# Kernel optimization log

Hardware: AMD Instinct MI355X
Metric: run time of the kernel (lower is better)

Reference implementation:

```python
import jax, jax.numpy as jnp
import numpy as np

K = 3  # kernel_dim
PAD = 1


def setup_inputs() -> dict:
    key = jax.random.key(0)
    ks = jax.random.split(key, 7)
    B, C_in, C_out, R = 2, 32, 64, 64
    H = W = D = 64
    return {
        "x": jax.random.normal(ks[0], (B, C_in, H, W, D), dtype=jnp.float32),
        "U_k_h": jax.random.normal(ks[1], (K, R), dtype=jnp.float32),
        "U_k_w": jax.random.normal(ks[2], (K, R), dtype=jnp.float32),
        "U_k_d": jax.random.normal(ks[3], (K, R), dtype=jnp.float32),
        "U_c_in": jax.random.normal(ks[4], (C_in, R), dtype=jnp.float32),
        "U_c_out": jax.random.normal(ks[5], (R, C_out), dtype=jnp.float32),
        "bias": jax.random.normal(ks[6], (C_out,), dtype=jnp.float32),
    }


def _cpd_conv3d(x, U_k_h, U_k_w, U_k_d, U_c_in, U_c_out, bias):
    # Equivalent to: patches[b,c,h,w,d,kh,kw,kd] contracted with
    # U_c_in[c,r] U_k_h[kh,r] U_k_w[kw,r] U_k_d[kd,r] U_c_out[r,co]
    # -> out[b,co,h,w,d].  We exploit the CP (rank-separable) structure
    # instead of materializing the unfolded patch tensor.
    xp = jnp.pad(x, ((0, 0), (0, 0), (PAD, PAD), (PAD, PAD), (PAD, PAD)))
    # channel contraction: [B, R, H+2, W+2, D+2]
    t = jnp.einsum('bchwd,cr->brhwd', xp, U_c_in)
    B, R, Hp, Wp, Dp = t.shape
    H, W, D = Hp - 2 * PAD, Wp - 2 * PAD, Dp - 2 * PAD
    # separable kernel contractions (fixed K=3 unrolled loops)
    t = sum(t[:, :, k:k + H, :, :] * U_k_h[k][None, :, None, None, None] for k in range(K))
    t = sum(t[:, :, :, k:k + W, :] * U_k_w[k][None, :, None, None, None] for k in range(K))
    t = sum(t[:, :, :, :, k:k + D] * U_k_d[k][None, :, None, None, None] for k in range(K))
    out = jnp.einsum('brhwd,rc->bchwd', t, U_c_out)
    return out + bias[None, :, None, None, None]


def reference(x, U_k_h, U_k_w, U_k_d, U_c_in, U_c_out, bias):
    return _cpd_conv3d(x, U_k_h, U_k_w, U_k_d, U_c_in, U_c_out, bias)
```

## Files before the change

kernel.cpp:

```cpp
#include <hip/hip_runtime.h>
#include <hip/hip_bf16.h>

typedef __attribute__((ext_vector_type(8))) short short8;
typedef __attribute__((ext_vector_type(4))) float f32x4;

__device__ __forceinline__ float b2f(short s) {
    return __uint_as_float(((unsigned int)(unsigned short)s) << 16);
}
__device__ __forceinline__ float b2f_lo(unsigned u) {
    return __uint_as_float(u << 16);
}
__device__ __forceinline__ float b2f_hi(unsigned u) {
    return __uint_as_float(u & 0xffff0000u);
}
__device__ __forceinline__ short f2b(float f) {
    union { __hip_bfloat16 h; short s; } cv;
    cv.h = __float2bfloat16(f);
    return cv.s;
}
__device__ __forceinline__ unsigned pack2(float a, float b) {
    union { __hip_bfloat162 h; unsigned u; } cv;
    cv.h = __float22bfloat162_rn(make_float2(a, b));
    return cv.u;
}

__global__ __launch_bounds__(64)
void k0_prep(const float* __restrict__ Uco, const float* __restrict__ Ucin,
             short* __restrict__ ucotT, short* __restrict__ ucinT)
{
    const int i = blockIdx.x * 64 + threadIdx.x;
    if (i < 4096) {
        int co = i >> 6, r = i & 63;
        ucotT[co * 64 + r] = f2b(Uco[r * 64 + co]);
    } else {
        int j = i - 4096;
        int r = j >> 5, c = j & 31;
        ucinT[r * 32 + c] = f2b(Ucin[c * 64 + r]);
    }
}

__global__ __launch_bounds__(256)
void k1_channel(const float* __restrict__ x,
                const float* __restrict__ Ucin,
                const short* __restrict__ ucinT_g,
                short* __restrict__ t)
{
    __shared__ short xs[256 * 32];
    __shared__ short uci[64 * 32];

    const int tid = threadIdx.x;
    const int gp0 = blockIdx.x * 256;
    const int b   = gp0 >> 18;
    const int sp  = (gp0 & 262143) + tid;
    const float* xp = x + ((long)b << 23) + sp;

    if (ucinT_g) {
        ((short8*)uci)[tid] = ((const short8*)ucinT_g)[tid];
    } else {
        for (int i = tid; i < 2048; i += 256) {
            int r = i >> 5, c = i & 31;
            uci[i] = f2b(Ucin[c * 64 + r]);
        }
    }

    {
        float v[32];
#pragma unroll
        for (int c = 0; c < 32; ++c) v[c] = xp[(long)c << 18];
        const int swz = (tid >> 1) & 3;
#pragma unroll
        for (int oct = 0; oct < 4; ++oct) {
            uint4 o;
            o.x = pack2(v[oct * 8 + 0], v[oct * 8 + 1]);
            o.y = pack2(v[oct * 8 + 2], v[oct * 8 + 3]);
            o.z = pack2(v[oct * 8 + 4], v[oct * 8 + 5]);
            o.w = pack2(v[oct * 8 + 6], v[oct * 8 + 7]);
            *(uint4*)&xs[tid * 32 + ((oct ^ swz) << 3)] = o;
        }
    }
    __syncthreads();

    const int lane = tid & 63, wv = tid >> 6;
    const int l15 = lane & 15, quad = lane >> 4;

    short8 afr[4];
#pragma unroll
    for (int mt = 0; mt < 4; ++mt)
        afr[mt] = *(const short8*)&uci[(mt * 16 + l15) * 32 + quad * 8];

    f32x4 acc[4][4] = {};
#pragma unroll
    for (int nt = 0; nt < 4; ++nt) {
        const int srow = wv * 64 + nt * 16 + l15;
        const int slot = quad ^ ((srow >> 1) & 3);
        short8 bfr = *(const short8*)&xs[srow * 32 + (slot << 3)];
#pragma unroll
        for (int mt = 0; mt < 4; ++mt)
            acc[mt][nt] = __builtin_amdgcn_mfma_f32_16x16x32_bf16(
                afr[mt], bfr, acc[mt][nt], 0, 0, 0);
    }

#pragma unroll
    for (int nt = 0; nt < 4; ++nt) {
        const int srow = wv * 64 + nt * 16 + l15;
        short* tb = t + ((size_t)(gp0 + srow) << 6);
#pragma unroll
        for (int mt = 0; mt < 4; ++mt) {
            uint2 o;
            o.x = pack2(acc[mt][nt][0], acc[mt][nt][1]);
            o.y = pack2(acc[mt][nt][2], acc[mt][nt][3]);
            *(uint2*)&tb[mt * 16 + quad * 4] = o;
        }
    }
}

__global__ __launch_bounds__(256)
void k2_conv_gemm(const short* __restrict__ t,
                  const float* __restrict__ Ukh,
                  const float* __restrict__ Ukw,
                  const float* __restrict__ Ukd,
                  const float* __restrict__ Uco,
                  const float* __restrict__ bias,
                  const short* __restrict__ ucotT,
                  float* __restrict__ out)
{
    __shared__ short s[66 * 64];
    __shared__ short p[64 * 72];
    __shared__ short ucot[64 * 72];

    const int tid = threadIdx.x;

    const int bid  = blockIdx.x;
    const int slot = bid & 7;
    const int idx  = bid >> 3;
    const int b    = idx >> 9;
    const int rem  = idx & 511;
    const int h    = slot * 8 + (rem >> 6);
    const int w    = rem & 63;

    const short* colp[9];
    bool valid[9];
#pragma unroll
    for (int kh = 0; kh < 3; ++kh) {
#pragma unroll
        for (int kw = 0; kw < 3; ++kw) {
            int hh = h + kh - 1, ww = w + kw - 1;
            bool v = ((unsigned)hh < 64u) && ((unsigned)ww < 64u);
            valid[kh * 3 + kw] = v;
            long base = v ? ((long)(b * 262144 + hh * 4096 + ww * 64) << 6) : 0;
            colp[kh * 3 + kw] = t + base;
        }
    }

    if (ucotT) {
        for (int i = tid; i < 512; i += 256) {
            int co = i >> 3, rb = i & 7;
            short8 v = *(const short8*)&ucotT[co * 64 + rb * 8];
            *(short8*)&ucot[co * 72 + rb * 8] = v;
        }
    } else {
        for (int i = tid; i < 4096; i += 256) {
            int r = i >> 6, co = i & 63;
            ucot[co * 72 + r] = f2b(Uco[i]);
        }
    }

    const int rq = tid & 15;
    float4 W[9];
    {
        float4 a[3], c[3];
#pragma unroll
        for (int k = 0; k < 3; ++k) {
            a[k] = *(const float4*)&Ukh[k * 64 + 4 * rq];
            c[k] = *(const float4*)&Ukw[k * 64 + 4 * rq];
        }
#pragma unroll
        for (int kh = 0; kh < 3; ++kh)
#pragma unroll
            for (int kw = 0; kw < 3; ++kw) {
                int kk = kh * 3 + kw;
                float m = valid[kk] ? 1.f : 0.f;
                W[kk].x = a[kh].x * c[kw].x * m;
                W[kk].y = a[kh].y * c[kw].y * m;
                W[kk].z = a[kh].z * c[kw].z * m;
                W[kk].w = a[kh].w * c[kw].w * m;
            }
    }

    if (tid < 32) {
        int sd = (tid < 16) ? 0 : 65;
        int rr = tid & 15;
        uint2 z; z.x = 0u; z.y = 0u;
        *(uint2*)&s[sd * 64 + 4 * rr] = z;
    }

#define PA_COMPUTE(BUF, J)                                                  \
    {                                                                       \
        float a0 = 0.f, a1 = 0.f, a2 = 0.f, a3 = 0.f;                       \
        _Pragma("unroll")                                                   \
        for (int kk = 0; kk < 9; ++kk) {                                    \
            uint2 uu = BUF[kk];                                             \
            a0 += W[kk].x * b2f_lo(uu.x);                                   \
            a1 += W[kk].y * b2f_hi(uu.x);                                   \
            a2 += W[kk].z * b2f_lo(uu.y);                                   \
            a3 += W[kk].w * b2f_hi(uu.y);                                   \
        }                                                                   \
        int sd = 1 + (tid >> 4) + 16 * (J);                                 \
        uint2 o; o.x = pack2(a0, a1); o.y = pack2(a2, a3);                  \
        *(uint2*)&s[sd * 64 + 4 * rq] = o;                                  \
    }

    {
        const int off0 = (tid >> 4) * 64 + 4 * rq;
        uint2 bA[9], bB[9], bC[9];
#pragma unroll
        for (int kk = 0; kk < 9; ++kk) bA[kk] = *(const uint2*)(colp[kk] + off0);
#pragma unroll
        for (int kk = 0; kk < 9; ++kk) bB[kk] = *(const uint2*)(colp[kk] + off0 + 1024);

#pragma unroll
        for (int kk = 0; kk < 9; ++kk) bC[kk] = *(const uint2*)(colp[kk] + off0 + 2048);
        PA_COMPUTE(bA, 0)
#pragma unroll
        for (int kk = 0; kk < 9; ++kk) bA[kk] = *(const uint2*)(colp[kk] + off0 + 3072);
        PA_COMPUTE(bB, 1)
        PA_COMPUTE(bC, 2)
        PA_COMPUTE(bA, 3)
    }
#undef PA_COMPUTE
    __syncthreads();

    {
        float4 Wd[3];
#pragma unroll
        for (int k = 0; k < 3; ++k)
            Wd[k] = *(const float4*)&Ukd[k * 64 + 4 * rq];
        for (int u = tid; u < 64 * 16; u += 256) {
            int d = u >> 4;
            float a0 = 0.f, a1 = 0.f, a2 = 0.f, a3 = 0.f;
#pragma unroll
            for (int k = 0; k < 3; ++k) {
                uint2 uu = *(const uint2*)&s[(d + k) * 64 + 4 * rq];
                a0 += Wd[k].x * b2f_lo(uu.x);
                a1 += Wd[k].y * b2f_hi(uu.x);
                a2 += Wd[k].z * b2f_lo(uu.y);
                a3 += Wd[k].w * b2f_hi(uu.y);
            }
            uint2 o; o.x = pack2(a0, a1); o.y = pack2(a2, a3);
            *(uint2*)&p[d * 72 + 4 * rq] = o;
        }
    }
    __syncthreads();

    {
        const int lane = tid & 63, wv = tid >> 6;
        const int l15 = lane & 15, quad = lane >> 4;
        short8 afr0 = *(const short8*)&p[(wv * 16 + l15) * 72 + quad * 8];
        short8 afr1 = *(const short8*)&p[(wv * 16 + l15) * 72 + 32 + quad * 8];
        f32x4 acc[4] = {};
#pragma unroll
        for (int nt = 0; nt < 4; ++nt) {
            short8 b0 = *(const short8*)&ucot[(nt * 16 + l15) * 72 + quad * 8];
            short8 b1 = *(const short8*)&ucot[(nt * 16 + l15) * 72 + 32 + quad * 8];
            acc[nt] = __builtin_amdgcn_mfma_f32_16x16x32_bf16(afr0, b0, acc[nt], 0, 0, 0);
            acc[nt] = __builtin_amdgcn_mfma_f32_16x16x32_bf16(afr1, b1, acc[nt], 0, 0, 0);
        }
#pragma unroll
        for (int nt = 0; nt < 4; ++nt) {
            int co = nt * 16 + l15;
            float bs = bias[co];
            int d = wv * 16 + quad * 4;
            float4 o;
            o.x = acc[nt][0] + bs; o.y = acc[nt][1] + bs;
            o.z = acc[nt][2] + bs; o.w = acc[nt][3] + bs;
            long addr = ((long)(b * 64 + co) << 18) + (h << 12) + (w << 6) + d;
            *(float4*)&out[addr] = o;
        }
    }
}

#define NTH 512
#define NPADP 656
#define SMEM_BYTES ((NPADP*32 + NPADP*32 + 432*32 + 64*32 + 64*64)*2 + 576*4)

__global__ __launch_bounds__(NTH)
void cpd_conv3d_fused_fb(const float* __restrict__ x,
                         const float* __restrict__ Ukh,
                         const float* __restrict__ Ukw,
                         const float* __restrict__ Ukd,
                         const float* __restrict__ Ucin,
                         const float* __restrict__ Uco,
                         const float* __restrict__ bias,
                         float* __restrict__ out)
{
    extern __shared__ char smem[];
    short* xs   = (short*)smem;
    short* t0   = xs   + NPADP*32;
    short* t1   = t0   + NPADP*32;
    short* uct  = t1   + 432*32;
    short* ucot = uct  + 64*32;
    float* ukf  = (float*)(ucot + 64*64);

    const int tid  = threadIdx.x;
    const int lane = tid & 63;
    const int wv   = tid >> 6;
    const int l15  = lane & 15;
    const int quad = lane >> 4;
    const int rg   = tid & 3;

    const int bid = blockIdx.x;
    const int dt = bid & 3, wt = (bid >> 2) & 15, ht = (bid >> 6) & 15, b = bid >> 10;
    const int h0 = ht * 4, w0 = wt * 4, d0 = dt * 16;

    for (int i = tid; i < 576; i += NTH) {
        float v = (i < 192) ? Ukh[i] : (i < 384 ? Ukw[i - 192] : Ukd[i - 384]);
        ukf[i] = v;
    }
    for (int i = tid; i < 2048; i += NTH) {
        int r = i >> 5, c = i & 31;
        uct[i] = f2b(Ucin[c * 64 + r]);
    }
    for (int i = tid; i < 4096; i += NTH) {
        int co = i >> 6, r = i & 63;
        ucot[i] = f2b(Uco[r * 64 + co]);
    }
    for (int i = tid; i < NPADP * 32; i += NTH) {
        int pp = i >> 5, c = i & 31;
        float v = 0.f;
        if (pp < 648) {
            int ph = pp / 108, rem = pp - ph * 108;
            int pw = rem / 18, pd = rem - pw * 18;
            int gh = h0 + ph - 1, gw = w0 + pw - 1, gd = d0 + pd - 1;
            if ((unsigned)gh < 64u && (unsigned)gw < 64u && (unsigned)gd < 64u)
                v = x[((long)(b * 32 + c) << 18) + (gh << 12) + (gw << 6) + gd];
        }
        xs[i] = f2b(v);
    }
    __syncthreads();

    f32x4 acc[8] = {};

    for (int pass = 0; pass < 2; ++pass) {
        const int rbase = pass * 32;
        {
            const int nt = wv & 1;
            short8 bfrag = *(const short8*)&uct[(rbase + nt * 16 + l15) * 32 + quad * 8];
            for (int mt = (wv >> 1); mt <= 40; mt += 4) {
                short8 afrag = *(const short8*)&xs[(mt * 16 + l15) * 32 + quad * 8];
                f32x4 c = {};
                c = __builtin_amdgcn_mfma_f32_16x16x32_bf16(afrag, bfrag, c, 0, 0, 0);
                const int col = nt * 16 + l15;
#pragma unroll
                for (int i2 = 0; i2 < 4; ++i2)
                    t0[(mt * 16 + quad * 4 + i2) * 32 + col] = f2b(c[i2]);
            }
        }
        __syncthreads();
        {
            float wh[3][8];
#pragma unroll
            for (int k = 0; k < 3; ++k) {
                const float4* pp_ = (const float4*)&ukf[k * 64 + rbase + rg * 8];
                float4 u0 = pp_[0], u1 = pp_[1];
                wh[k][0]=u0.x; wh[k][1]=u0.y; wh[k][2]=u0.z; wh[k][3]=u0.w;
                wh[k][4]=u1.x; wh[k][5]=u1.y; wh[k][6]=u1.z; wh[k][7]=u1.w;
            }
            for (int item = tid; item < 1728; item += NTH) {
                int q = item >> 2;
                float v[8] = {};
#pragma unroll
                for (int k = 0; k < 3; ++k) {
                    short8 sv = *(const short8*)&t0[(q + k * 108) * 32 + rg * 8];
#pragma unroll
                    for (int j = 0; j < 8; ++j) v[j] += wh[k][j] * b2f(sv[j]);
                }
                short8 o;
#pragma unroll
                for (int j = 0; j < 8; ++j) o[j] = f2b(v[j]);
                *(short8*)&t1[q * 32 + rg * 8] = o;
            }
        }
        __syncthreads();
        {
            float ww[3][8];
#pragma unroll
            for (int k = 0; k < 3; ++k) {
                const float4* pp_ = (const float4*)&ukf[(3 + k) * 64 + rbase + rg * 8];
                float4 u0 = pp_[0], u1 = pp_[1];
                ww[k][0]=u0.x; ww[k][1]=u0.y; ww[k][2]=u0.z; ww[k][3]=u0.w;
                ww[k][4]=u1.x; ww[k][5]=u1.y; ww[k][6]=u1.z; ww[k][7]=u1.w;
            }
            for (int item = tid; item < 1152; item += NTH) {
                int q2 = item >> 2;
                int oh = q2 / 72;
                int src = q2 + oh * 36;
                float v[8] = {};
#pragma unroll
                for (int k = 0; k < 3; ++k) {
                    short8 sv = *(const short8*)&t1[(src + k * 18) * 32 + rg * 8];
#pragma unroll
                    for (int j = 0; j < 8; ++j) v[j] += ww[k][j] * b2f(sv[j]);
                }
                short8 o;
#pragma unroll
                for (int j = 0; j < 8; ++j) o[j] = f2b(v[j]);
                *(short8*)&t0[q2 * 32 + rg * 8] = o;
            }
        }
        __syncthreads();
        {
            float wd[3][8];
#pragma unroll
            for (int k = 0; k < 3; ++k) {
                const float4* pp_ = (const float4*)&ukf[(6 + k) * 64 + rbase + rg * 8];
                float4 u0 = pp_[0], u1 = pp_[1];
                wd[k][0]=u0.x; wd[k][1]=u0.y; wd[k][2]=u0.z; wd[k][3]=u0.w;
                wd[k][4]=u1.x; wd[k][5]=u1.y; wd[k][6]=u1.z; wd[k][7]=u1.w;
            }
            for (int item = tid; item < 1024; item += NTH) {
                int pq = item >> 2;
                int src = pq + (pq >> 4) * 2;
                float v[8] = {};
#pragma unroll
                for (int k = 0; k < 3; ++k) {
                    short8 sv = *(const short8*)&t0[(src + k) * 32 + rg * 8];
#pragma unroll
                    for (int j = 0; j < 8; ++j) v[j] += wd[k][j] * b2f(sv[j]);
                }
                short8 o;
#pragma unroll
                for (int j = 0; j < 8; ++j) o[j] = f2b(v[j]);
                *(short8*)&t1[pq * 32 + rg * 8] = o;
            }
        }
        __syncthreads();
        {
            short8 bfr[4];
#pragma unroll
            for (int nt = 0; nt < 4; ++nt)
                bfr[nt] = *(const short8*)&ucot[(nt * 16 + l15) * 64 + rbase + quad * 8];
#pragma unroll
            for (int i = 0; i < 8; ++i) {
                int mt = wv * 2 + (i >> 2), nt = i & 3;
                short8 afr = *(const short8*)&t1[(mt * 16 + l15) * 32 + quad * 8];
                acc[i] = __builtin_amdgcn_mfma_f32_16x16x32_bf16(afr, bfr[nt], acc[i], 0, 0, 0);
            }
        }
    }

#pragma unroll
    for (int i = 0; i < 8; ++i) {
        int mt = wv * 2 + (i >> 2), nt = i & 3;
        int co = nt * 16 + l15;
        int oh = mt >> 2, ow = mt & 3;
        float bs = bias[co];
        float4 o4;
        o4.x = acc[i][0] + bs; o4.y = acc[i][1] + bs;
        o4.z = acc[i][2] + bs; o4.w = acc[i][3] + bs;
        long addr = ((long)(b * 64 + co) << 18) + ((long)(h0 + oh) << 12)
                  + ((w0 + ow) << 6) + (d0 + quad * 4);
        *(float4*)&out[addr] = o4;
    }
}

extern "C" void kernel_launch(void* const* d_in, const int* in_sizes, int n_in,
                              void* d_out, int out_size, void* d_ws, size_t ws_size,
                              hipStream_t stream) {
    const float* x    = (const float*)d_in[0];
    const float* Ukh  = (const float*)d_in[1];
    const float* Ukw  = (const float*)d_in[2];
    const float* Ukd  = (const float*)d_in[3];
    const float* Ucin = (const float*)d_in[4];
    const float* Uco  = (const float*)d_in[5];
    const float* bias = (const float*)d_in[6];
    float* out = (float*)d_out;

    const size_t needT = (size_t)2 * 262144 * 64 * 2;
    const size_t needM = (4096 + 2048) * 2;
    if (ws_size >= needT) {
        short* t = (short*)d_ws;
        short* ucotT = nullptr;
        short* ucinT = nullptr;
        if (ws_size >= needT + needM) {
            ucotT = (short*)((char*)d_ws + needT);
            ucinT = ucotT + 4096;
            k0_prep<<<96, 64, 0, stream>>>(Uco, Ucin, ucotT, ucinT);
        }
        k1_channel<<<2048, 256, 0, stream>>>(x, Ucin, ucinT, t);
        k2_conv_gemm<<<8192, 256, 0, stream>>>(t, Ukh, Ukw, Ukd, Uco, bias, ucotT, out);
    } else {
        (void)hipFuncSetAttribute((const void*)cpd_conv3d_fused_fb,
                                  hipFuncAttributeMaxDynamicSharedMemorySize,
                                  SMEM_BYTES);
        cpd_conv3d_fused_fb<<<2048, NTH, SMEM_BYTES, stream>>>(
            x, Ukh, Ukw, Ukd, Ucin, Uco, bias, out);
    }
}
```

Before: 264.1 us.

## Fuse depth-axis conv into MFMA operand load and swizzle shared tile

Removes the separate depth-convolution pass that wrote an intermediate shared buffer p. The depth taps are now computed directly in registers while building the MFMA A fragments, which drops one __syncthreads and a round trip through shared memory. The s tile is stored with an XOR swizzle to avoid bank conflicts on the 16-byte row reads, and the Ukd weights are staged in shared memory. Each thread now does the depth FMAs for its own fragment rows, and the kernel needs less LDS, which could raise occupancy.

```diff
diff --git a/kernel.cpp b/kernel.cpp
--- a/kernel.cpp
+++ b/kernel.cpp
@@ -125,8 +125,8 @@
                   float* __restrict__ out)
 {
     __shared__ short s[66 * 64];
-    __shared__ short p[64 * 72];
     __shared__ short ucot[64 * 72];
+    __shared__ float ukds[192];
 
     const int tid = threadIdx.x;
 
@@ -152,6 +152,8 @@
         }
     }
 
+    if (tid < 192) ukds[tid] = Ukd[tid];
+
     if (ucotT) {
         for (int i = tid; i < 512; i += 256) {
             int co = i >> 3, rb = i & 7;
@@ -191,7 +193,7 @@
         int sd = (tid < 16) ? 0 : 65;
         int rr = tid & 15;
         uint2 z; z.x = 0u; z.y = 0u;
-        *(uint2*)&s[sd * 64 + 4 * rr] = z;
+        *(uint2*)((char*)s + sd * 128 + ((8 * rr) ^ ((sd & 7) << 4))) = z;
     }
 
 #define PA_COMPUTE(BUF, J)                                                  \
@@ -207,7 +209,7 @@
         }                                                                   \
         int sd = 1 + (tid >> 4) + 16 * (J);                                 \
         uint2 o; o.x = pack2(a0, a1); o.y = pack2(a2, a3);                  \
-        *(uint2*)&s[sd * 64 + 4 * rq] = o;                                  \
+        *(uint2*)((char*)s + sd * 128 + ((8 * rq) ^ ((sd & 7) << 4))) = o;  \
     }
 
     {
@@ -231,32 +233,38 @@
     __syncthreads();
 
     {
-        float4 Wd[3];
-#pragma unroll
-        for (int k = 0; k < 3; ++k)
-            Wd[k] = *(const float4*)&Ukd[k * 64 + 4 * rq];
-        for (int u = tid; u < 64 * 16; u += 256) {
-            int d = u >> 4;
-            float a0 = 0.f, a1 = 0.f, a2 = 0.f, a3 = 0.f;
-#pragma unroll
-            for (int k = 0; k < 3; ++k) {
-                uint2 uu = *(const uint2*)&s[(d + k) * 64 + 4 * rq];
-                a0 += Wd[k].x * b2f_lo(uu.x);
-                a1 += Wd[k].y * b2f_hi(uu.x);
-                a2 += Wd[k].z * b2f_lo(uu.y);
-                a3 += Wd[k].w * b2f_hi(uu.y);
-            }
-            uint2 o; o.x = pack2(a0, a1); o.y = pack2(a2, a3);
-            *(uint2*)&p[d * 72 + 4 * rq] = o;
-        }
-    }
-    __syncthreads();
-
-    {
         const int lane = tid & 63, wv = tid >> 6;
         const int l15 = lane & 15, quad = lane >> 4;
-        short8 afr0 = *(const short8*)&p[(wv * 16 + l15) * 72 + quad * 8];
-        short8 afr1 = *(const short8*)&p[(wv * 16 + l15) * 72 + 32 + quad * 8];
+        const int row0 = wv * 16 + l15;
+
+        float p0[8] = {}, p1[8] = {};
+#pragma unroll
+        for (int k = 0; k < 3; ++k) {
+            const int row = row0 + k;
+            const int swz = (row & 7) << 4;
+            const char* rb = (const char*)s + row * 128;
+            short8 sv0 = *(const short8*)(rb + ((quad * 16) ^ swz));
+            short8 sv1 = *(const short8*)(rb + ((64 + quad * 16) ^ swz));
+            float4 wa = *(const float4*)&ukds[k * 64 + quad * 8];
+            float4 wb = *(const float4*)&ukds[k * 64 + quad * 8 + 4];
+            float4 wc = *(const float4*)&ukds[k * 64 + 32 + quad * 8];
+            float4 wd = *(const float4*)&ukds[k * 64 + 32 + quad * 8 + 4];
+            p0[0] += wa.x * b2f(sv0[0]);  p0[1] += wa.y * b2f(sv0[1]);
+            p0[2] += wa.z * b2f(sv0[2]);  p0[3] += wa.w * b2f(sv0[3]);
+            p0[4] += wb.x * b2f(sv0[4]);  p0[5] += wb.y * b2f(sv0[5]);
+            p0[6] += wb.z * b2f(sv0[6]);  p0[7] += wb.w * b2f(sv0[7]);
+            p1[0] += wc.x * b2f(sv1[0]);  p1[1] += wc.y * b2f(sv1[1]);
+            p1[2] += wc.z * b2f(sv1[2]);  p1[3] += wc.w * b2f(sv1[3]);
+            p1[4] += wd.x * b2f(sv1[4]);  p1[5] += wd.y * b2f(sv1[5]);
+            p1[6] += wd.z * b2f(sv1[6]);  p1[7] += wd.w * b2f(sv1[7]);
+        }
+        union { short8 s8; unsigned u[4]; } a0c, a1c;
+        a0c.u[0] = pack2(p0[0], p0[1]); a0c.u[1] = pack2(p0[2], p0[3]);
+        a0c.u[2] = pack2(p0[4], p0[5]); a0c.u[3] = pack2(p0[6], p0[7]);
+        a1c.u[0] = pack2(p1[0], p1[1]); a1c.u[1] = pack2(p1[2], p1[3]);
+        a1c.u[2] = pack2(p1[4], p1[5]); a1c.u[3] = pack2(p1[6], p1[7]);
+        short8 afr0 = a0c.s8, afr1 = a1c.s8;
+
         f32x4 acc[4] = {};
 #pragma unroll
         for (int nt = 0; nt < 4; ++nt) {
```

New measurement: 260.3 us. About the same (-1.4%).
